# Optimization experiments

Measured on AMD Instinct MI355X. Metric: run time of the kernel, lower is better.

## Reference

```python
import jax, jax.numpy as jnp
import numpy as np

N = 100000
E = 3200000
D = 64


def setup_inputs() -> dict:
    key = jax.random.key(0)
    k1, k2, k3 = jax.random.split(key, 3)
    indices = jax.random.randint(k1, (2, E), 0, N, dtype=jnp.int64) if jax.config.jax_enable_x64 else jax.random.randint(k1, (2, E), 0, N, dtype=jnp.int32)
    values = jax.random.uniform(k2, (E,), dtype=jnp.float32)
    b = jax.random.normal(k3, (N, D), dtype=jnp.float32)
    return {"indices": indices, "values": values, "shape": N, "b": b}


def reference(indices, values, shape, b):
    # sparse COO [N,N] @ dense [N,D]:
    # out[r] = sum over edges e with row[e]==r of values[e] * b[col[e]]
    row, col = indices[0], indices[1]
    msgs = values[:, None] * b[col]            # [E, D] gather + scale
    out = jax.ops.segment_sum(msgs, row, num_segments=shape)  # [N, D] scatter-add
    return out
```

## Files before the change

kernel.cpp:

```cpp
#include <hip/hip_runtime.h>
#include <hip/hip_bf16.h>


#define D 64
#define BROWS 64
#define MAXNB 2048
#define CAP 2560
#define NM (CAP / 256)
#define SPILLCAP 8192
#define NCHUNK 8
#define NBINS (BROWS * NCHUNK)

#define CROWS 2048
#define NCB 64
#define SCH_A 2048
#define CBLK 4352
#define NBLK_C 16
#define CAPC (CBLK * NBLK_C)

#define SCH 4096

__global__ __launch_bounds__(256) void spmm_atomic_kernel(
    const int* __restrict__ rows, const int* __restrict__ cols,
    const float* __restrict__ vals, const float* __restrict__ b,
    float* __restrict__ out, int E) {
  long long gid = (long long)blockIdx.x * blockDim.x + threadIdx.x;
  int e = (int)(gid >> 6);
  int d = (int)(gid & 63);
  if (e >= E) return;
  atomicAdd(&out[(long long)rows[e] * D + d], vals[e] * b[(long long)cols[e] * D + d]);
}

__device__ __forceinline__ unsigned bf16rne(float x) {
  unsigned u = __float_as_uint(x);
  return (u + 0x7FFFu + ((u >> 16) & 1u)) >> 16;
}
__global__ __launch_bounds__(256) void convert_kernel(
    const float4* __restrict__ src, uint2* __restrict__ dst, int n4) {
  int i = blockIdx.x * 256 + threadIdx.x;
  if (i >= n4) return;
  float4 f = src[i];
  dst[i] = make_uint2(bf16rne(f.x) | (bf16rne(f.y) << 16),
                      bf16rne(f.z) | (bf16rne(f.w) << 16));
}

__global__ __launch_bounds__(256) void coarse_scatter_kernel(
    const int* __restrict__ rows, const int* __restrict__ cols,
    const float* __restrict__ vals, int* __restrict__ gcoarse,
    uint2* __restrict__ cslab_lo, uint2* __restrict__ cslab_hi, int csplit,
    uint4* __restrict__ spill, int* __restrict__ spill_cnt, int E) {
  __shared__ uint2 stage[SCH_A];
  __shared__ unsigned char sbin[SCH_A];
  __shared__ int h[NCB];
  __shared__ int lst[NCB];
  __shared__ int gb[NCB];
  int t = threadIdx.x;
  if (t < NCB) h[t] = 0;
  __syncthreads();
  int start = blockIdx.x * SCH_A;
  int ec = E - start;
  if (ec > SCH_A) ec = SCH_A;

  int bin[8];
  int rank[8];
  unsigned key[8];
  float vv[8];
#pragma unroll
  for (int ki = 0; ki < 2; ki++) {
    int e0 = start + ki * 1024 + t * 4;
    int j0 = ki * 4;
    if (e0 + 3 < E) {
      int4 r = ((const int4*)(rows + start + ki * 1024))[t];
      int4 c = ((const int4*)(cols + start + ki * 1024))[t];
      float4 v = ((const float4*)(vals + start + ki * 1024))[t];
      int rl[4] = {r.x, r.y, r.z, r.w};
      int cl[4] = {c.x, c.y, c.z, c.w};
      float vl[4] = {v.x, v.y, v.z, v.w};
#pragma unroll
      for (int j = 0; j < 4; j++) {
        int bn = rl[j] >> 11;
        bin[j0 + j] = bn;
        rank[j0 + j] = atomicAdd(&h[bn], 1);
        key[j0 + j] = ((unsigned)(rl[j] & (CROWS - 1)) << 17) | (unsigned)cl[j];
        vv[j0 + j] = vl[j];
      }
    } else {
#pragma unroll
      for (int j = 0; j < 4; j++) {
        int e = e0 + j;
        bin[j0 + j] = -1;
        if (e < E) {
          int r = rows[e];
          int bn = r >> 11;
          bin[j0 + j] = bn;
          rank[j0 + j] = atomicAdd(&h[bn], 1);
          key[j0 + j] = ((unsigned)(r & (CROWS - 1)) << 17) | (unsigned)cols[e];
          vv[j0 + j] = vals[e];
        }
      }
    }
  }
  __syncthreads();
  if (t < NCB) {
    int c = h[t];
    int x = c;
#pragma unroll
    for (int off = 1; off < 64; off <<= 1) {
      int u = __shfl_up(x, off);
      if (t >= off) x += u;
    }
    lst[t] = x - c;
    gb[t] = c ? atomicAdd(&gcoarse[t], c) : 0;
  }
  __syncthreads();
#pragma unroll
  for (int j = 0; j < 8; j++) {
    if (bin[j] >= 0) {
      int pos = lst[bin[j]] + rank[j];
      stage[pos] = make_uint2(key[j], __float_as_uint(vv[j]));
      sbin[pos] = (unsigned char)bin[j];
    }
  }
  __syncthreads();
  for (int i = t; i < ec; i += 256) {
    int bn = sbin[i];
    uint2 p = stage[i];
    int pin = gb[bn] + (i - lst[bn]);
    if (pin < CAPC) {
      uint2* slab = (bn < csplit) ? (cslab_lo + (size_t)bn * CAPC)
                                  : (cslab_hi + (size_t)(bn - csplit) * CAPC);
      slab[pin] = p;
    } else {
      int sp = atomicAdd(spill_cnt, 1);
      if (sp < SPILLCAP)
        spill[sp] = make_uint4((unsigned)((bn << 11) | (int)(p.x >> 17)),
                               p.x & 0x1FFFFu, p.y, 0u);
    }
  }
}

__global__ __launch_bounds__(256) void fine_scatter_kernel(
    const int* __restrict__ gcoarse, const uint2* __restrict__ cslab_lo,
    const uint2* __restrict__ cslab_hi, int csplit, int* __restrict__ gcount,
    uint2* __restrict__ pairs, uint4* __restrict__ spill,
    int* __restrict__ spill_cnt) {
  int c = blockIdx.x >> 4;
  int blk = blockIdx.x & 15;
  int cnt = gcoarse[c];
  if (cnt > CAPC) cnt = CAPC;
  int base = blk * CBLK;
  int ec = cnt - base;
  if (ec <= 0) return;
  if (ec > CBLK) ec = CBLK;
  const uint2* src = ((c < csplit) ? (cslab_lo + (size_t)c * CAPC)
                                   : (cslab_hi + (size_t)(c - csplit) * CAPC)) +
                     base;
  __shared__ uint2 stage[CBLK];
  __shared__ unsigned char sbin[CBLK];
  __shared__ int h[32];
  __shared__ int lst[32];
  __shared__ int gb[32];
  int t = threadIdx.x;
  if (t < 32) h[t] = 0;
  __syncthreads();
  int rank[17];
#pragma unroll
  for (int k = 0; k < 17; k++) {
    int i = k * 256 + t;
    if (i < ec) rank[k] = atomicAdd(&h[src[i].x >> 23], 1);
  }
  __syncthreads();
  if (t < 32) {
    int cn = h[t];
    int x = cn;
#pragma unroll
    for (int off = 1; off < 32; off <<= 1) {
      int u = __shfl_up(x, off);
      if (t >= off) x += u;
    }
    lst[t] = x - cn;
    gb[t] = cn ? atomicAdd(&gcount[c * 32 + t], cn) : 0;
  }
  __syncthreads();
#pragma unroll
  for (int k = 0; k < 17; k++) {
    int i = k * 256 + t;
    if (i < ec) {
      uint2 p = src[i];
      int f = (int)(p.x >> 23);
      int pos = lst[f] + rank[k];
      unsigned key2 = (((p.x >> 17) & 63u) << 26) | ((p.x & 0x1FFFFu) << 7);
      stage[pos] = make_uint2(key2, p.y);
      sbin[pos] = (unsigned char)f;
    }
  }
  __syncthreads();
  for (int i = t; i < ec; i += 256) {
    int f = sbin[i];
    uint2 p = stage[i];
    int pin = gb[f] + (i - lst[f]);
    int gbkt = c * 32 + f;
    if (pin < CAP) {
      pairs[(size_t)gbkt * CAP + pin] = p;
    } else {
      int sp = atomicAdd(spill_cnt, 1);
      if (sp < SPILLCAP)
        spill[sp] = make_uint4((unsigned)(gbkt * 64 + (int)(p.x >> 26)),
                               (p.x >> 7) & 0x1FFFFu, p.y, 0u);
    }
  }
}

__global__ __launch_bounds__(256) void binned_scatter_kernel(
    const int* __restrict__ rows, const int* __restrict__ cols,
    const float* __restrict__ vals, int* __restrict__ gcount,
    uint2* __restrict__ pairs, uint4* __restrict__ spill,
    int* __restrict__ spill_cnt, int E, int NB) {
  __shared__ int h[MAXNB];
  __shared__ int baseoff[MAXNB];
  int t = threadIdx.x;
  for (int i = t; i < NB; i += 256) h[i] = 0;
  __syncthreads();
  int start = blockIdx.x * SCH;
  bool full = (start + SCH <= E);
  int4 r4[4];
  int rank[16];
  if (full) {
#pragma unroll
    for (int ki = 0; ki < 4; ki++) {
      r4[ki] = ((const int4*)(rows + start + ki * 1024))[t];
      rank[4 * ki + 0] = atomicAdd(&h[r4[ki].x >> 6], 1);
      rank[4 * ki + 1] = atomicAdd(&h[r4[ki].y >> 6], 1);
      rank[4 * ki + 2] = atomicAdd(&h[r4[ki].z >> 6], 1);
      rank[4 * ki + 3] = atomicAdd(&h[r4[ki].w >> 6], 1);
    }
  } else {
#pragma unroll
    for (int ki = 0; ki < 4; ki++) {
      int e = start + ki * 1024 + t * 4;
      int4 rr = make_int4(0, 0, 0, 0);
      if (e + 0 < E) { rr.x = rows[e + 0]; rank[4 * ki + 0] = atomicAdd(&h[rr.x >> 6], 1); }
      if (e + 1 < E) { rr.y = rows[e + 1]; rank[4 * ki + 1] = atomicAdd(&h[rr.y >> 6], 1); }
      if (e + 2 < E) { rr.z = rows[e + 2]; rank[4 * ki + 2] = atomicAdd(&h[rr.z >> 6], 1); }
      if (e + 3 < E) { rr.w = rows[e + 3]; rank[4 * ki + 3] = atomicAdd(&h[rr.w >> 6], 1); }
      r4[ki] = rr;
    }
  }
  __syncthreads();
  for (int i = t; i < NB; i += 256)
    baseoff[i] = h[i] ? atomicAdd(&gcount[i], h[i]) : 0;
  __syncthreads();
#pragma unroll
  for (int ki = 0; ki < 4; ki++) {
    int e = start + ki * 1024 + t * 4;
    int cc[4], rr[4] = {r4[ki].x, r4[ki].y, r4[ki].z, r4[ki].w};
    float vv[4];
    if (full) {
      int4 c4 = ((const int4*)(cols + start + ki * 1024))[t];
      float4 v4 = ((const float4*)(vals + start + ki * 1024))[t];
      cc[0] = c4.x; cc[1] = c4.y; cc[2] = c4.z; cc[3] = c4.w;
      vv[0] = v4.x; vv[1] = v4.y; vv[2] = v4.z; vv[3] = v4.w;
    } else {
#pragma unroll
      for (int j = 0; j < 4; j++) {
        cc[j] = (e + j < E) ? cols[e + j] : 0;
        vv[j] = (e + j < E) ? vals[e + j] : 0.f;
      }
    }
#pragma unroll
    for (int j = 0; j < 4; j++) {
      if (e + j < E) {
        int r = rr[j];
        int bk = r >> 6;
        int pin = baseoff[bk] + rank[4 * ki + j];
        if (pin < CAP) {
          unsigned key = ((unsigned)(r & (BROWS - 1)) << 26) |
                         ((unsigned)cc[j] << 7);
          pairs[(size_t)bk * CAP + pin] = make_uint2(key, __float_as_uint(vv[j]));
        } else {
          int sp = atomicAdd(spill_cnt, 1);
          if (sp < SPILLCAP)
            spill[sp] = make_uint4((unsigned)r, (unsigned)cc[j],
                                   __float_as_uint(vv[j]), 0u);
        }
      }
    }
  }
}

__global__ __launch_bounds__(256) void spmm_fused_kernel(
    const uint2* __restrict__ pairs, const int* __restrict__ gcount,
    const uint2* __restrict__ b16, float* __restrict__ out, int N) {
  __shared__ uint2 lp[CAP];
  __shared__ int cnt[NBINS];
  __shared__ int roff[NBINS + 1];
  __shared__ int wpart[4];
  int bkt = blockIdx.x;
  int cntE = gcount[bkt];
  if (cntE > CAP) cntE = CAP;
  const uint2* src = pairs + (size_t)bkt * CAP;
  int t = threadIdx.x;
  int lane = t & 63;
  int wv = t >> 6;
  for (int i = t; i < NBINS; i += 256) cnt[i] = 0;
  __syncthreads();
  uint2 mine[NM];
  int rk[NM];
#pragma unroll
  for (int k = 0; k < NM; k++) {
    int i = t + k * 256;
    if (i < cntE) {
      mine[k] = src[i];
      int bin = ((mine[k].x >> 26) << 3) | ((mine[k].x >> 21) & 7);
      rk[k] = atomicAdd(&cnt[bin], 1);
    }
  }
  __syncthreads();
  {
    int c0 = cnt[2 * t];
    int c1 = cnt[2 * t + 1];
    int s = c0 + c1;
    int x = s;
#pragma unroll
    for (int off = 1; off < 64; off <<= 1) {
      int u = __shfl_up(x, off);
      if (lane >= off) x += u;
    }
    if (lane == 63) wpart[wv] = x;
    __syncthreads();
    int wbase = 0;
    for (int w = 0; w < wv; w++) wbase += wpart[w];
    int thoff = wbase + x - s;
    roff[2 * t] = thoff;
    roff[2 * t + 1] = thoff + c0;
    if (t == 255) roff[NBINS] = wbase + x;
  }
  __syncthreads();
#pragma unroll
  for (int k = 0; k < NM; k++) {
    int i = t + k * 256;
    if (i < cntE) {
      int bin = ((mine[k].x >> 26) << 3) | ((mine[k].x >> 21) & 7);
      lp[roff[bin] + rk[k]] = make_uint2(mine[k].x & 0x03FFFF80u, mine[k].y);
    }
  }
  __syncthreads();
  int g = lane >> 3;
  int l8 = lane & 7;
  int gid32 = wv * 8 + g;
  const char* bq = (const char*)b16 + (l8 << 4);
  int row_base = bkt * BROWS;
  float acc[2][8] = {{0.f, 0.f, 0.f, 0.f, 0.f, 0.f, 0.f, 0.f},
                     {0.f, 0.f, 0.f, 0.f, 0.f, 0.f, 0.f, 0.f}};
  for (int ch = 0; ch < NCHUNK; ch++) {
#pragma unroll
    for (int rr = 0; rr < 2; rr++) {
      int r = gid32 + 32 * rr;
      int bin = (r << 3) | ch;
      int j0 = roff[bin], j1 = roff[bin + 1];
      for (int base = j0; base < j1; base += 4) {
        uint4 bv[4];
        float vv[4];
#pragma unroll
        for (int k = 0; k < 4; k++) {
          int idx = base + k;
          int ic = (idx < j1) ? idx : j0;
          uint2 p = lp[ic];
          bv[k] = *(const uint4*)(bq + p.x);
          vv[k] = (idx < j1) ? __uint_as_float(p.y) : 0.f;
        }
#pragma unroll
        for (int k = 0; k < 4; k++) {
          unsigned u0 = bv[k].x, u1 = bv[k].y, u2 = bv[k].z, u3 = bv[k].w;
          float v = vv[k];
          acc[rr][0] += v * __uint_as_float(u0 << 16);
          acc[rr][1] += v * __uint_as_float(u0 & 0xFFFF0000u);
          acc[rr][2] += v * __uint_as_float(u1 << 16);
          acc[rr][3] += v * __uint_as_float(u1 & 0xFFFF0000u);
          acc[rr][4] += v * __uint_as_float(u2 << 16);
          acc[rr][5] += v * __uint_as_float(u2 & 0xFFFF0000u);
          acc[rr][6] += v * __uint_as_float(u3 << 16);
          acc[rr][7] += v * __uint_as_float(u3 & 0xFFFF0000u);
        }
      }
    }
  }
#pragma unroll
  for (int rr = 0; rr < 2; rr++) {
    int gr = row_base + gid32 + 32 * rr;
    if (gr < N) {
      float4* dst = (float4*)(out + (size_t)gr * D + l8 * 8);
      dst[0] = make_float4(acc[rr][0], acc[rr][1], acc[rr][2], acc[rr][3]);
      dst[1] = make_float4(acc[rr][4], acc[rr][5], acc[rr][6], acc[rr][7]);
    }
  }
}

__global__ __launch_bounds__(256) void spill_fix_kernel(
    const uint4* __restrict__ spill, const int* __restrict__ spill_cnt,
    const float* __restrict__ b, float* __restrict__ out) {
  int n = *spill_cnt;
  if (n > SPILLCAP) n = SPILLCAP;
  int lane = threadIdx.x & 63;
  int w = (int)((blockIdx.x * blockDim.x + threadIdx.x) >> 6);
  int nw = (int)((gridDim.x * blockDim.x) >> 6);
  for (int s = w; s < n; s += nw) {
    uint4 e = spill[s];
    atomicAdd(&out[(size_t)e.x * D + lane],
              __uint_as_float(e.z) * b[(size_t)e.y * D + lane]);
  }
}

extern "C" void kernel_launch(void* const* d_in, const int* in_sizes, int n_in,
                              void* d_out, int out_size, void* d_ws, size_t ws_size,
                              hipStream_t stream) {
  const int* indices = (const int*)d_in[0];
  const float* vals  = (const float*)d_in[1];
  const float* b     = (const float*)d_in[3];

  int E = in_sizes[1];
  int N = in_sizes[3] / D;
  const int* rows = indices;
  const int* cols = indices + E;

  int NB = (N + BROWS - 1) / BROWS;
  int NC = (N + CROWS - 1) / CROWS;
  int n4 = N * D / 4;

  size_t off_gcount  = 0;
  size_t off_gcoarse = off_gcount + (size_t)MAXNB * 4;
  size_t off_scnt    = off_gcoarse + (size_t)NCB * 4;
  size_t off_spill   = (off_scnt + 4 + 15) & ~(size_t)15;
  size_t off_pairs   = off_spill + (size_t)SPILLCAP * 16;
  size_t npbkt       = (size_t)NC * 32;
  size_t off_b16     = off_pairs + npbkt * CAP * 8;
  size_t off_cextra  = off_b16 + (size_t)N * D * 2;
  size_t outbytes    = (size_t)out_size * 4;
  int csplit = (int)(outbytes / ((size_t)CAPC * 8));
  if (csplit > NC) csplit = NC;
  size_t cextra = (size_t)(NC - csplit) * CAPC * 8;
  size_t need2 = off_cextra + cextra;

  if (ws_size >= need2 && NC <= NCB && (int)npbkt <= MAXNB && NB <= MAXNB) {
    char*  ws        = (char*)d_ws;
    int*   gcount    = (int*)(ws + off_gcount);
    int*   gcoarse   = (int*)(ws + off_gcoarse);
    int*   spill_cnt = (int*)(ws + off_scnt);
    uint4* spill     = (uint4*)(ws + off_spill);
    uint2* pairs     = (uint2*)(ws + off_pairs);
    uint2* b16       = (uint2*)(ws + off_b16);
    uint2* cslab_lo  = (uint2*)d_out;
    uint2* cslab_hi  = (uint2*)(ws + off_cextra);

    hipMemsetAsync(gcount, 0, (size_t)MAXNB * 4 + (size_t)NCB * 4 + 4, stream);
    convert_kernel<<<(n4 + 255) / 256, 256, 0, stream>>>(
        (const float4*)b, b16, n4);
    coarse_scatter_kernel<<<(E + SCH_A - 1) / SCH_A, 256, 0, stream>>>(
        rows, cols, vals, gcoarse, cslab_lo, cslab_hi, csplit,
        spill, spill_cnt, E);
    fine_scatter_kernel<<<NC * NBLK_C, 256, 0, stream>>>(
        gcoarse, cslab_lo, cslab_hi, csplit, gcount, pairs, spill, spill_cnt);
    spmm_fused_kernel<<<NB, 256, 0, stream>>>(pairs, gcount, b16,
                                              (float*)d_out, N);
    spill_fix_kernel<<<16, 256, 0, stream>>>(spill, spill_cnt, b,
                                             (float*)d_out);
    return;
  }

  size_t l_gcount = 0;
  size_t l_scnt   = l_gcount + (size_t)NB * 4;
  size_t l_spill  = (l_scnt + 4 + 15) & ~(size_t)15;
  size_t l_pairs  = (l_spill + (size_t)SPILLCAP * 16 + 15) & ~(size_t)15;
  size_t l_b16    = l_pairs + (size_t)NB * CAP * 8;
  size_t need1    = l_b16 + (size_t)N * D * 2;

  if (ws_size < need1 || NB > MAXNB) {
    hipMemsetAsync(d_out, 0, (size_t)out_size * sizeof(float), stream);
    long long total = (long long)E * 64;
    spmm_atomic_kernel<<<(int)((total + 255) / 256), 256, 0, stream>>>(
        rows, cols, vals, b, (float*)d_out, E);
    return;
  }

  char*  ws        = (char*)d_ws;
  int*   gcount    = (int*)(ws + l_gcount);
  int*   spill_cnt = (int*)(ws + l_scnt);
  uint4* spill     = (uint4*)(ws + l_spill);
  uint2* pairs     = (uint2*)(ws + l_pairs);
  uint2* b16       = (uint2*)(ws + l_b16);

  hipMemsetAsync(gcount, 0, (size_t)NB * 4 + 4, stream);
  convert_kernel<<<(n4 + 255) / 256, 256, 0, stream>>>(
      (const float4*)b, b16, n4);
  int scat_blocks = (E + SCH - 1) / SCH;
  binned_scatter_kernel<<<scat_blocks, 256, 0, stream>>>(
      rows, cols, vals, gcount, pairs, spill, spill_cnt, E, NB);
  spmm_fused_kernel<<<NB, 256, 0, stream>>>(pairs, gcount, b16,
                                            (float*)d_out, N);
  spill_fix_kernel<<<16, 256, 0, stream>>>(spill, spill_cnt, b, (float*)d_out);
}
```

Before: 228.9 us.

## Halve column chunks, double coarse-scatter chunk, and cache slab loads in registers

Result: faster. 219.3 us (-4.2%).

```diff
diff --git a/kernel.cpp b/kernel.cpp
--- a/kernel.cpp
+++ b/kernel.cpp
@@ -8,12 +8,12 @@
 #define CAP 2560
 #define NM (CAP / 256)
 #define SPILLCAP 8192
-#define NCHUNK 8
+#define NCHUNK 4
 #define NBINS (BROWS * NCHUNK)
 
 #define CROWS 2048
 #define NCB 64
-#define SCH_A 2048
+#define SCH_A 4096
 #define CBLK 4352
 #define NBLK_C 16
 #define CAPC (CBLK * NBLK_C)
@@ -60,44 +60,29 @@
   int start = blockIdx.x * SCH_A;
   int ec = E - start;
   if (ec > SCH_A) ec = SCH_A;
-
-  int bin[8];
-  int rank[8];
-  unsigned key[8];
-  float vv[8];
-#pragma unroll
-  for (int ki = 0; ki < 2; ki++) {
-    int e0 = start + ki * 1024 + t * 4;
-    int j0 = ki * 4;
-    if (e0 + 3 < E) {
-      int4 r = ((const int4*)(rows + start + ki * 1024))[t];
-      int4 c = ((const int4*)(cols + start + ki * 1024))[t];
-      float4 v = ((const float4*)(vals + start + ki * 1024))[t];
-      int rl[4] = {r.x, r.y, r.z, r.w};
-      int cl[4] = {c.x, c.y, c.z, c.w};
-      float vl[4] = {v.x, v.y, v.z, v.w};
-#pragma unroll
-      for (int j = 0; j < 4; j++) {
-        int bn = rl[j] >> 11;
-        bin[j0 + j] = bn;
-        rank[j0 + j] = atomicAdd(&h[bn], 1);
-        key[j0 + j] = ((unsigned)(rl[j] & (CROWS - 1)) << 17) | (unsigned)cl[j];
-        vv[j0 + j] = vl[j];
-      }
-    } else {
-#pragma unroll
-      for (int j = 0; j < 4; j++) {
-        int e = e0 + j;
-        bin[j0 + j] = -1;
-        if (e < E) {
-          int r = rows[e];
-          int bn = r >> 11;
-          bin[j0 + j] = bn;
-          rank[j0 + j] = atomicAdd(&h[bn], 1);
-          key[j0 + j] = ((unsigned)(r & (CROWS - 1)) << 17) | (unsigned)cols[e];
-          vv[j0 + j] = vals[e];
-        }
-      }
+  bool full = (start + SCH_A <= E);
+
+  int4 r4[4];
+  int rank[16];
+  if (full) {
+#pragma unroll
+    for (int ki = 0; ki < 4; ki++) {
+      r4[ki] = ((const int4*)(rows + start + ki * 1024))[t];
+      rank[4 * ki + 0] = atomicAdd(&h[r4[ki].x >> 11], 1);
+      rank[4 * ki + 1] = atomicAdd(&h[r4[ki].y >> 11], 1);
+      rank[4 * ki + 2] = atomicAdd(&h[r4[ki].z >> 11], 1);
+      rank[4 * ki + 3] = atomicAdd(&h[r4[ki].w >> 11], 1);
+    }
+  } else {
+#pragma unroll
+    for (int ki = 0; ki < 4; ki++) {
+      int e = start + ki * 1024 + t * 4;
+      int4 rr = make_int4(-1, -1, -1, -1);
+      if (e + 0 < E) { rr.x = rows[e + 0]; rank[4 * ki + 0] = atomicAdd(&h[rr.x >> 11], 1); }
+      if (e + 1 < E) { rr.y = rows[e + 1]; rank[4 * ki + 1] = atomicAdd(&h[rr.y >> 11], 1); }
+      if (e + 2 < E) { rr.z = rows[e + 2]; rank[4 * ki + 2] = atomicAdd(&h[rr.z >> 11], 1); }
+      if (e + 3 < E) { rr.w = rows[e + 3]; rank[4 * ki + 3] = atomicAdd(&h[rr.w >> 11], 1); }
+      r4[ki] = rr;
     }
   }
   __syncthreads();
@@ -114,11 +99,34 @@
   }
   __syncthreads();
 #pragma unroll
-  for (int j = 0; j < 8; j++) {
-    if (bin[j] >= 0) {
-      int pos = lst[bin[j]] + rank[j];
-      stage[pos] = make_uint2(key[j], __float_as_uint(vv[j]));
-      sbin[pos] = (unsigned char)bin[j];
+  for (int ki = 0; ki < 4; ki++) {
+    int e = start + ki * 1024 + t * 4;
+    int rr[4] = {r4[ki].x, r4[ki].y, r4[ki].z, r4[ki].w};
+    int cc[4];
+    float vv[4];
+    if (full) {
+      int4 c4 = ((const int4*)(cols + start + ki * 1024))[t];
+      float4 v4 = ((const float4*)(vals + start + ki * 1024))[t];
+      cc[0] = c4.x; cc[1] = c4.y; cc[2] = c4.z; cc[3] = c4.w;
+      vv[0] = v4.x; vv[1] = v4.y; vv[2] = v4.z; vv[3] = v4.w;
+    } else {
+#pragma unroll
+      for (int j = 0; j < 4; j++) {
+        cc[j] = (e + j < E) ? cols[e + j] : 0;
+        vv[j] = (e + j < E) ? vals[e + j] : 0.f;
+      }
+    }
+#pragma unroll
+    for (int j = 0; j < 4; j++) {
+      if (e + j < E) {
+        int r = rr[j];
+        int bn = r >> 11;
+        int pos = lst[bn] + rank[4 * ki + j];
+        stage[pos] = make_uint2(((unsigned)(r & (CROWS - 1)) << 17) |
+                                    (unsigned)cc[j],
+                                __float_as_uint(vv[j]));
+        sbin[pos] = (unsigned char)bn;
+      }
     }
   }
   __syncthreads();
@@ -163,11 +171,15 @@
   int t = threadIdx.x;
   if (t < 32) h[t] = 0;
   __syncthreads();
+  uint2 mine[17];
   int rank[17];
 #pragma unroll
   for (int k = 0; k < 17; k++) {
     int i = k * 256 + t;
-    if (i < ec) rank[k] = atomicAdd(&h[src[i].x >> 23], 1);
+    if (i < ec) {
+      mine[k] = src[i];
+      rank[k] = atomicAdd(&h[mine[k].x >> 23], 1);
+    }
   }
   __syncthreads();
   if (t < 32) {
@@ -186,7 +198,7 @@
   for (int k = 0; k < 17; k++) {
     int i = k * 256 + t;
     if (i < ec) {
-      uint2 p = src[i];
+      uint2 p = mine[k];
       int f = (int)(p.x >> 23);
       int pos = lst[f] + rank[k];
       unsigned key2 = (((p.x >> 17) & 63u) << 26) | ((p.x & 0x1FFFFu) << 7);
@@ -302,7 +314,7 @@
   int t = threadIdx.x;
   int lane = t & 63;
   int wv = t >> 6;
-  for (int i = t; i < NBINS; i += 256) cnt[i] = 0;
+  if (t < NBINS) cnt[t] = 0;
   __syncthreads();
   uint2 mine[NM];
   int rk[NM];
@@ -311,16 +323,14 @@
     int i = t + k * 256;
     if (i < cntE) {
       mine[k] = src[i];
-      int bin = ((mine[k].x >> 26) << 3) | ((mine[k].x >> 21) & 7);
+      int bin = ((mine[k].x >> 26) << 2) | ((mine[k].x >> 22) & 3);
       rk[k] = atomicAdd(&cnt[bin], 1);
     }
   }
   __syncthreads();
   {
-    int c0 = cnt[2 * t];
-    int c1 = cnt[2 * t + 1];
-    int s = c0 + c1;
-    int x = s;
+    int c0 = cnt[t];
+    int x = c0;
 #pragma unroll
     for (int off = 1; off < 64; off <<= 1) {
       int u = __shfl_up(x, off);
@@ -330,9 +340,7 @@
     __syncthreads();
     int wbase = 0;
     for (int w = 0; w < wv; w++) wbase += wpart[w];
-    int thoff = wbase + x - s;
-    roff[2 * t] = thoff;
-    roff[2 * t + 1] = thoff + c0;
+    roff[t] = wbase + x - c0;
     if (t == 255) roff[NBINS] = wbase + x;
   }
   __syncthreads();
@@ -340,7 +348,7 @@
   for (int k = 0; k < NM; k++) {
     int i = t + k * 256;
     if (i < cntE) {
-      int bin = ((mine[k].x >> 26) << 3) | ((mine[k].x >> 21) & 7);
+      int bin = ((mine[k].x >> 26) << 2) | ((mine[k].x >> 22) & 3);
       lp[roff[bin] + rk[k]] = make_uint2(mine[k].x & 0x03FFFF80u, mine[k].y);
     }
   }
@@ -356,7 +364,7 @@
 #pragma unroll
     for (int rr = 0; rr < 2; rr++) {
       int r = gid32 + 32 * rr;
-      int bin = (r << 3) | ch;
+      int bin = (r << 2) | ch;
       int j0 = roff[bin], j1 = roff[bin + 1];
       for (int base = j0; base < j1; base += 4) {
         uint4 bv[4];
```
